# Kernel tuning notes

Hardware: AMD Instinct MI355X
Metric: run time of the kernel (lower is better)

## Reference

```python
import jax, jax.numpy as jnp
import numpy as np

B, C, H, W = 4, 64, 64, 64
CQK = C // 8


def setup_inputs() -> dict:
    key = jax.random.key(0)
    ks = jax.random.split(key, 4)
    x = jax.random.normal(ks[0], (B, C, H, W), dtype=jnp.float32)
    Wq = jax.random.normal(ks[1], (CQK, C), dtype=jnp.float32) * (1.0 / np.sqrt(C))
    bq = jnp.zeros((CQK,), dtype=jnp.float32)
    Wk = jax.random.normal(ks[2], (CQK, C), dtype=jnp.float32) * (1.0 / np.sqrt(C))
    bk = jnp.zeros((CQK,), dtype=jnp.float32)
    Wv = jax.random.normal(ks[3], (C, C), dtype=jnp.float32) * (1.0 / np.sqrt(C))
    bv = jnp.zeros((C,), dtype=jnp.float32)
    gamma = jnp.ones((1,), dtype=jnp.float32)
    return {"x": x, "Wq": Wq, "bq": bq, "Wk": Wk, "bk": bk,
            "Wv": Wv, "bv": bv, "gamma": gamma}


def reference(x, Wq, bq, Wk, bk, Wv, bv, gamma):
    b, c, h, w = x.shape
    n = h * w
    xf = x.reshape(b, c, n)                      # [B, C, N]
    # 1x1 convs == per-pixel linear over channels
    q = jnp.einsum('oc,bcn->bon', Wq, xf) + bq[:, None]   # [B, C/8, N]
    k = jnp.einsum('oc,bcn->bon', Wk, xf) + bk[:, None]   # [B, C/8, N]
    v = jnp.einsum('oc,bcn->bon', Wv, xf) + bv[:, None]   # [B, C, N]
    # attention_map[b,i,j] = <q[:, i], k[:, j]>; softmax over j
    attn = jax.nn.softmax(jnp.einsum('bci,bcj->bij', q, k), axis=-1)  # [B, N, N]
    # out[b,c,i] = sum_j v[b,c,j] * attn[b,i,j]  (bmm(V, attn^T))
    out = jnp.einsum('bcj,bij->bci', v, attn).reshape(b, c, h, w)
    return gamma * out + x
```

## Files before the change

### kernel.cpp

```cpp
#include <hip/hip_runtime.h>
#include <hip/hip_bf16.h>
#include <math.h>

#define NPIX 4096

typedef __attribute__((ext_vector_type(8))) short s8;
typedef __attribute__((ext_vector_type(4))) short s4;
typedef __attribute__((ext_vector_type(16))) float f16v;

static __device__ __forceinline__ unsigned packbf2(float a, float b) {
    union { __hip_bfloat162 h; unsigned u; } x;
    x.h = __float22bfloat162_rn(make_float2(a, b));
    return x.u;
}
static __device__ __forceinline__ float fexp2(float x) {
#if __has_builtin(__builtin_amdgcn_exp2f)
    return __builtin_amdgcn_exp2f(x);
#else
    return exp2f(x);
#endif
}

__global__ __launch_bounds__(256) void prep_kernel(
    const float* __restrict__ x,
    const float* __restrict__ Wq, const float* __restrict__ bq,
    const float* __restrict__ Wk, const float* __restrict__ bk,
    __hip_bfloat16* __restrict__ qbf, __hip_bfloat16* __restrict__ kbf,
    __hip_bfloat16* __restrict__ xbf)
{
    __shared__ float Xp[64][65];
    int t = threadIdx.x;
    int lane = t & 63;
    int grp  = t >> 6;
    int b  = blockIdx.x >> 6;
    int n0 = (blockIdx.x & 63) << 6;

    const float* xb = x + ((size_t)b << 18);
    __hip_bfloat16* xbb = xbf + ((size_t)b << 18);
#pragma unroll
    for (int u = 0; u < 16; ++u) {
        int c = grp + u * 4;
        float v = xb[((size_t)c << 12) + n0 + lane];
        Xp[c][lane] = v;
        xbb[((size_t)c << 12) + n0 + lane] = __float2bfloat16(v);
    }
    __syncthreads();

    int o0 = grp * 2, o1 = o0 + 1;
    float qa0 = bq[o0], qa1 = bq[o1], ka0 = bk[o0], ka1 = bk[o1];
    const float* wq0 = Wq + o0 * 64; const float* wq1 = Wq + o1 * 64;
    const float* wk0 = Wk + o0 * 64; const float* wk1 = Wk + o1 * 64;
#pragma unroll
    for (int c = 0; c < 64; ++c) {
        float xv = Xp[c][lane];
        qa0 = fmaf(wq0[c], xv, qa0);
        qa1 = fmaf(wq1[c], xv, qa1);
        ka0 = fmaf(wk0[c], xv, ka0);
        ka1 = fmaf(wk1[c], xv, ka1);
    }
    qa0 *= 1.4426950408889634f;
    qa1 *= 1.4426950408889634f;
    int pix = b * NPIX + n0 + lane;
    *(__hip_bfloat162*)(qbf + (size_t)pix * 8 + o0) =
        __float22bfloat162_rn(make_float2(qa0, qa1));
    *(__hip_bfloat162*)(kbf + (size_t)pix * 8 + o0) =
        __float22bfloat162_rn(make_float2(ka0, ka1));
}

__global__ __launch_bounds__(512, 4) void flash_fused_kernel(
    const __hip_bfloat16* __restrict__ qbf, const __hip_bfloat16* __restrict__ kbf,
    const __hip_bfloat16* __restrict__ xbf,
    const float* __restrict__ Wv, const float* __restrict__ bv,
    const float* __restrict__ x, const float* __restrict__ gamma,
    float* __restrict__ out)
{
    __shared__ __align__(16) char pool[35200];
    unsigned short* Xs = (unsigned short*)pool;

    int t = threadIdx.x;
    int w    = t >> 6;
    int lane = t & 63;
    int l32  = lane & 31;
    int lh   = lane >> 5;

    int b  = blockIdx.x >> 7;
    int i0 = (blockIdx.x & 127) << 5;

    const s8 zero8 = {0, 0, 0, 0, 0, 0, 0, 0};

    s8 qf;
    {
        s8 qv = *(const s8*)(qbf + ((size_t)(b * NPIX + i0 + l32) << 3));
        qf = (lh == 0) ? qv : zero8;
    }

    f16v acc[2];
    f16v zero16;
#pragma unroll
    for (int r = 0; r < 16; ++r) { acc[0][r] = 0.f; acc[1][r] = 0.f; zero16[r] = 0.f; }
    float lsum = 0.f;

    const __hip_bfloat16* kb = kbf + ((size_t)(b * NPIX) << 3);
    const unsigned short* xg = (const unsigned short*)xbf + ((size_t)b << 18);

    int c = t >> 3, seg = t & 7;
    const unsigned short* xsrc = xg + ((size_t)c << 12) + seg * 32;
    int xdst = c * 260 + seg * 32;

    uint2 pv[8];
    s8 kf;
    {
        const unsigned short* p = xsrc;
#pragma unroll
        for (int u = 0; u < 8; ++u) pv[u] = *(const uint2*)(p + u * 4);
        kf = *(const s8*)(kb + ((size_t)(w * 32 + l32) << 3));
    }

    for (int jt = 0; jt < 16; ++jt) {
        __syncthreads();

        {
            unsigned short* dstp = Xs + xdst;
#pragma unroll
            for (int u = 0; u < 8; ++u) *(uint2*)(dstp + u * 4) = pv[u];
        }

        f16v sC = __builtin_amdgcn_mfma_f32_32x32x16_bf16(kf, qf, zero16, 0, 0, 0);
        float e[16];
#pragma unroll
        for (int r = 0; r < 16; ++r) e[r] = fexp2(sC[r]);
#pragma unroll
        for (int r = 0; r < 16; ++r) lsum += e[r];
        unsigned P2[8];
#pragma unroll
        for (int s = 0; s < 8; ++s) P2[s] = packbf2(e[2 * s], e[2 * s + 1]);

        __syncthreads();

        {
            int jn = ((jt + 1) & 15) << 8;
            const unsigned short* p = xsrc + jn;
#pragma unroll
            for (int u = 0; u < 8; ++u) pv[u] = *(const uint2*)(p + u * 4);
            kf = *(const s8*)(kb + ((size_t)(jn + w * 32 + l32) << 3));
        }

#if __has_builtin(__builtin_amdgcn_mfma_f32_32x32x8bf16_1k)
#pragma unroll
        for (int cm = 0; cm < 2; ++cm) {
            const unsigned short* xrow = Xs + (cm * 32 + l32) * 260 + w * 32 + lh * 4;
#pragma unroll
            for (int q = 0; q < 4; ++q) {
                s4 xf = *(const s4*)(xrow + q * 8);
                union { uint2 u; s4 v; } pu;
                pu.u.x = P2[2 * q]; pu.u.y = P2[2 * q + 1];
                acc[cm] = __builtin_amdgcn_mfma_f32_32x32x8bf16_1k(xf, pu.v, acc[cm], 0, 0, 0);
            }
        }
#else
        {
            unsigned X0 = __shfl_xor(P2[0], 32), X1 = __shfl_xor(P2[1], 32);
            unsigned X2 = __shfl_xor(P2[2], 32), X3 = __shfl_xor(P2[3], 32);
            unsigned X4 = __shfl_xor(P2[4], 32), X5 = __shfl_xor(P2[5], 32);
            unsigned X6 = __shfl_xor(P2[6], 32), X7 = __shfl_xor(P2[7], 32);
            union { uint4 u[2]; s8 v[2]; } bf;
            bf.u[0].x = lh ? X2 : P2[0]; bf.u[0].y = lh ? X3 : P2[1];
            bf.u[0].z = lh ? P2[2] : X0; bf.u[0].w = lh ? P2[3] : X1;
            bf.u[1].x = lh ? X6 : P2[4]; bf.u[1].y = lh ? X7 : P2[5];
            bf.u[1].z = lh ? P2[6] : X4; bf.u[1].w = lh ? P2[7] : X5;
#pragma unroll
            for (int cm = 0; cm < 2; ++cm) {
                const unsigned short* xrow = Xs + (cm * 32 + l32) * 260 + w * 32 + lh * 8;
#pragma unroll
                for (int q = 0; q < 2; ++q) {
                    union { uint2 u[2]; s8 v; } xu;
                    xu.u[0] = *(const uint2*)(xrow + q * 16);
                    xu.u[1] = *(const uint2*)(xrow + q * 16 + 4);
                    acc[cm] = __builtin_amdgcn_mfma_f32_32x32x16_bf16(xu.v, bf.v[q], acc[cm], 0, 0, 0);
                }
            }
        }
#endif
    }

    float* OshA = (float*)pool;
    float* OshB = (float*)(pool + 8704);
    float* Linv = (float*)(pool + 17408);
    float* bvs  = (float*)(pool + 17536);
    float* Wvs  = (float*)(pool + 17792);
    float* Lsh  = (float*)(pool + 34176);

    lsum += __shfl_xor(lsum, 32);
    if (lh == 0) Lsh[w * 32 + l32] = lsum;

    float* Og = (w >> 2) ? OshB : OshA;
    for (int s = 0; s < 4; ++s) {
        __syncthreads();
        if ((w & 3) == s) {
#pragma unroll
            for (int cm = 0; cm < 2; ++cm)
#pragma unroll
                for (int r = 0; r < 16; ++r) {
                    int cc = cm * 32 + (r & 3) + 8 * (r >> 2) + 4 * lh;
                    float* p = Og + l32 * 68 + cc;
                    if (s == 0) *p = acc[cm][r];
                    else        *p += acc[cm][r];
                }
        }
    }
    __syncthreads();

    if (t < 32) {
        float lt = 0.f;
#pragma unroll
        for (int ww = 0; ww < 8; ++ww) lt += Lsh[ww * 32 + t];
        Linv[t] = 1.0f / lt;
    }
    if (t < 64) bvs[t] = bv[t];
    {
        const float4* wsrc = (const float4*)Wv;
        float4* wdst = (float4*)Wvs;
        wdst[t] = wsrc[t];
        wdst[t + 512] = wsrc[t + 512];
    }
    __syncthreads();

    {
        int i  = t & 31;
        int cg = t >> 5;
        float inv = Linv[i];
        float res[4] = {0.f, 0.f, 0.f, 0.f};
#pragma unroll 4
        for (int cb = 0; cb < 16; ++cb) {
            float4 oa = *(const float4*)(OshA + i * 68 + cb * 4);
            float4 ob = *(const float4*)(OshB + i * 68 + cb * 4);
            float4 o = make_float4(oa.x + ob.x, oa.y + ob.y, oa.z + ob.z, oa.w + ob.w);
#pragma unroll
            for (int k = 0; k < 4; ++k) {
                const float4 wv4 = *(const float4*)(Wvs + (cg * 4 + k) * 64 + cb * 4);
                res[k] = fmaf(wv4.x, o.x, fmaf(wv4.y, o.y, fmaf(wv4.z, o.z, fmaf(wv4.w, o.w, res[k]))));
            }
        }
        float g = gamma[0];
        const float* xr = x + ((size_t)b << 18) + i0;
        float* outp = out + ((size_t)b << 18) + i0;
#pragma unroll
        for (int k = 0; k < 4; ++k) {
            int cch = cg * 4 + k;
            float attn = fmaf(res[k], inv, bvs[cch]);
            size_t off = ((size_t)cch << 12) + i;
            outp[off] = fmaf(g, attn, xr[off]);
        }
    }
}

extern "C" void kernel_launch(void* const* d_in, const int* in_sizes, int n_in,
                              void* d_out, int out_size, void* d_ws, size_t ws_size,
                              hipStream_t stream) {
    const float* x     = (const float*)d_in[0];
    const float* Wq    = (const float*)d_in[1];
    const float* bq    = (const float*)d_in[2];
    const float* Wk    = (const float*)d_in[3];
    const float* bk    = (const float*)d_in[4];
    const float* Wv    = (const float*)d_in[5];
    const float* bv    = (const float*)d_in[6];
    const float* gamma = (const float*)d_in[7];
    float* out = (float*)d_out;

    __hip_bfloat16* qbf = (__hip_bfloat16*)d_ws;
    __hip_bfloat16* kbf = qbf + (size_t)4 * NPIX * 8;
    __hip_bfloat16* xbf = kbf + (size_t)4 * NPIX * 8;

    prep_kernel<<<256, 256, 0, stream>>>(x, Wq, bq, Wk, bk, qbf, kbf, xbf);
    flash_fused_kernel<<<512, 512, 0, stream>>>(qbf, kbf, xbf, Wv, bv, x, gamma, out);
}
```

Baseline: 109.5 us.

## Double-buffer X tiles with XOR swizzle and permlane32 swap for PV MFMA

Replaces the single padded shared-memory X tile with two swizzled 32KB buffers, so each iteration needs one barrier instead of two. Global prefetch now runs two tiles ahead, using 16-byte loads and stores. The P·V product uses the 32x32x16 bf16 MFMA, with operands rearranged through permlane32_swap in place of the older 32x32x8 path. This raises LDS use to 64KB per block, which may cut occupancy below the four blocks requested in launch bounds.

```diff
diff --git a/kernel.cpp b/kernel.cpp
--- a/kernel.cpp
+++ b/kernel.cpp
@@ -5,7 +5,6 @@
 #define NPIX 4096
 
 typedef __attribute__((ext_vector_type(8))) short s8;
-typedef __attribute__((ext_vector_type(4))) short s4;
 typedef __attribute__((ext_vector_type(16))) float f16v;
 
 static __device__ __forceinline__ unsigned packbf2(float a, float b) {
@@ -18,6 +17,19 @@
     return __builtin_amdgcn_exp2f(x);
 #else
     return exp2f(x);
+#endif
+}
+
+static __device__ __forceinline__ void lane_swap(unsigned a, unsigned b, int lh,
+                                                 unsigned &x, unsigned &y) {
+#if __has_builtin(__builtin_amdgcn_permlane32_swap)
+    auto r = __builtin_amdgcn_permlane32_swap((int)a, (int)b, false, false);
+    x = (unsigned)r[0];
+    y = (unsigned)r[1];
+#else
+    unsigned sa = __shfl_xor(a, 32), sb = __shfl_xor(b, 32);
+    x = lh ? sb : a;
+    y = lh ? b : sa;
 #endif
 }
 
@@ -74,8 +86,9 @@
     const float* __restrict__ x, const float* __restrict__ gamma,
     float* __restrict__ out)
 {
-    __shared__ __align__(16) char pool[35200];
-    unsigned short* Xs = (unsigned short*)pool;
+    __shared__ __align__(16) char pool[65536];
+    unsigned short* Xs0 = (unsigned short*)pool;
+    unsigned short* Xs1 = (unsigned short*)(pool + 32768);
 
     int t = threadIdx.x;
     int w    = t >> 6;
@@ -103,29 +116,46 @@
     const __hip_bfloat16* kb = kbf + ((size_t)(b * NPIX) << 3);
     const unsigned short* xg = (const unsigned short*)xbf + ((size_t)b << 18);
 
-    int c = t >> 3, seg = t & 7;
-    const unsigned short* xsrc = xg + ((size_t)c << 12) + seg * 32;
-    int xdst = c * 260 + seg * 32;
-
-    uint2 pv[8];
-    s8 kf;
-    {
-        const unsigned short* p = xsrc;
-#pragma unroll
-        for (int u = 0; u < 8; ++u) pv[u] = *(const uint2*)(p + u * 4);
-        kf = *(const s8*)(kb + ((size_t)(w * 32 + l32) << 3));
-    }
-
-    for (int jt = 0; jt < 16; ++jt) {
-        __syncthreads();
-
-        {
-            unsigned short* dstp = Xs + xdst;
-#pragma unroll
-            for (int u = 0; u < 8; ++u) *(uint2*)(dstp + u * 4) = pv[u];
+    int crow = (t & 7) + (w << 3);
+    int seg  = (t >> 3) & 7;
+    int cx   = crow & 7;
+    const unsigned short* xsrc = xg + ((size_t)crow << 12) + seg * 32;
+    int wrow = crow * 256;
+
+    int c7    = l32 & 7;
+    int gbase = 4 * w + lh;
+    int woff  = w * 32 + l32;
+
+    uint4 pv[4];
+    s8 kfA, kfB;
+
+#pragma unroll
+    for (int u = 0; u < 4; ++u) pv[u] = *(const uint4*)(xsrc + u * 8);
+    kfA = *(const s8*)(kb + ((size_t)(0 * 256 + woff) << 3));
+    kfB = *(const s8*)(kb + ((size_t)(1 * 256 + woff) << 3));
+#pragma unroll
+    for (int u = 0; u < 4; ++u)
+        *(uint4*)(Xs0 + wrow + ((((seg << 2) + u) ^ cx) << 3)) = pv[u];
+#pragma unroll
+    for (int u = 0; u < 4; ++u) pv[u] = *(const uint4*)(xsrc + 256 + u * 8);
+    __syncthreads();
+
+    auto body = [&](int jt, const unsigned short* XsC, unsigned short* XsN, s8& kf) {
+        if (jt < 15) {
+#pragma unroll
+            for (int u = 0; u < 4; ++u)
+                *(uint4*)(XsN + wrow + ((((seg << 2) + u) ^ cx) << 3)) = pv[u];
         }
 
         f16v sC = __builtin_amdgcn_mfma_f32_32x32x16_bf16(kf, qf, zero16, 0, 0, 0);
+
+        if (jt < 14) {
+#pragma unroll
+            for (int u = 0; u < 4; ++u)
+                pv[u] = *(const uint4*)(xsrc + (jt + 2) * 256 + u * 8);
+            kf = *(const s8*)(kb + ((size_t)((jt + 2) * 256 + woff) << 3));
+        }
+
         float e[16];
 #pragma unroll
         for (int r = 0; r < 16; ++r) e[r] = fexp2(sC[r]);
@@ -135,52 +165,35 @@
 #pragma unroll
         for (int s = 0; s < 8; ++s) P2[s] = packbf2(e[2 * s], e[2 * s + 1]);
 
+        unsigned b00, b01, b02, b03, b10, b11, b12, b13;
+        lane_swap(P2[0], P2[2], lh, b00, b02);
+        lane_swap(P2[1], P2[3], lh, b01, b03);
+        lane_swap(P2[4], P2[6], lh, b10, b12);
+        lane_swap(P2[5], P2[7], lh, b11, b13);
+        union { unsigned u[4]; s8 v; } bf0, bf1;
+        bf0.u[0] = b00; bf0.u[1] = b01; bf0.u[2] = b02; bf0.u[3] = b03;
+        bf1.u[0] = b10; bf1.u[1] = b11; bf1.u[2] = b12; bf1.u[3] = b13;
+
+        {
+            const unsigned short* xb0 = XsC + l32 * 256;
+            const unsigned short* xb1 = XsC + (32 + l32) * 256;
+            s8 xf;
+            xf = *(const s8*)(xb0 + (((gbase + 0) ^ c7) << 3));
+            acc[0] = __builtin_amdgcn_mfma_f32_32x32x16_bf16(xf, bf0.v, acc[0], 0, 0, 0);
+            xf = *(const s8*)(xb0 + (((gbase + 2) ^ c7) << 3));
+            acc[0] = __builtin_amdgcn_mfma_f32_32x32x16_bf16(xf, bf1.v, acc[0], 0, 0, 0);
+            xf = *(const s8*)(xb1 + (((gbase + 0) ^ c7) << 3));
+            acc[1] = __builtin_amdgcn_mfma_f32_32x32x16_bf16(xf, bf0.v, acc[1], 0, 0, 0);
+            xf = *(const s8*)(xb1 + (((gbase + 2) ^ c7) << 3));
+            acc[1] = __builtin_amdgcn_mfma_f32_32x32x16_bf16(xf, bf1.v, acc[1], 0, 0, 0);
+        }
+
         __syncthreads();
-
-        {
-            int jn = ((jt + 1) & 15) << 8;
-            const unsigned short* p = xsrc + jn;
-#pragma unroll
-            for (int u = 0; u < 8; ++u) pv[u] = *(const uint2*)(p + u * 4);
-            kf = *(const s8*)(kb + ((size_t)(jn + w * 32 + l32) << 3));
-        }
-
-#if __has_builtin(__builtin_amdgcn_mfma_f32_32x32x8bf16_1k)
-#pragma unroll
-        for (int cm = 0; cm < 2; ++cm) {
-            const unsigned short* xrow = Xs + (cm * 32 + l32) * 260 + w * 32 + lh * 4;
-#pragma unroll
-            for (int q = 0; q < 4; ++q) {
-                s4 xf = *(const s4*)(xrow + q * 8);
-                union { uint2 u; s4 v; } pu;
-                pu.u.x = P2[2 * q]; pu.u.y = P2[2 * q + 1];
-                acc[cm] = __builtin_amdgcn_mfma_f32_32x32x8bf16_1k(xf, pu.v, acc[cm], 0, 0, 0);
-            }
-        }
-#else
-        {
-            unsigned X0 = __shfl_xor(P2[0], 32), X1 = __shfl_xor(P2[1], 32);
-            unsigned X2 = __shfl_xor(P2[2], 32), X3 = __shfl_xor(P2[3], 32);
-            unsigned X4 = __shfl_xor(P2[4], 32), X5 = __shfl_xor(P2[5], 32);
-            unsigned X6 = __shfl_xor(P2[6], 32), X7 = __shfl_xor(P2[7], 32);
-            union { uint4 u[2]; s8 v[2]; } bf;
-            bf.u[0].x = lh ? X2 : P2[0]; bf.u[0].y = lh ? X3 : P2[1];
-            bf.u[0].z = lh ? P2[2] : X0; bf.u[0].w = lh ? P2[3] : X1;
-            bf.u[1].x = lh ? X6 : P2[4]; bf.u[1].y = lh ? X7 : P2[5];
-            bf.u[1].z = lh ? P2[6] : X4; bf.u[1].w = lh ? P2[7] : X5;
-#pragma unroll
-            for (int cm = 0; cm < 2; ++cm) {
-                const unsigned short* xrow = Xs + (cm * 32 + l32) * 260 + w * 32 + lh * 8;
-#pragma unroll
-                for (int q = 0; q < 2; ++q) {
-                    union { uint2 u[2]; s8 v; } xu;
-                    xu.u[0] = *(const uint2*)(xrow + q * 16);
-                    xu.u[1] = *(const uint2*)(xrow + q * 16 + 4);
-                    acc[cm] = __builtin_amdgcn_mfma_f32_32x32x16_bf16(xu.v, bf.v[q], acc[cm], 0, 0, 0);
-                }
-            }
-        }
-#endif
+    };
+
+    for (int jt = 0; jt < 16; jt += 2) {
+        body(jt,     Xs0, Xs1, kfA);
+        body(jt + 1, Xs1, Xs0, kfB);
     }
 
     float* OshA = (float*)pool;
```

After: 154.9 us. 1.41x slower.
